# Optimization experiments

Hardware: AMD Instinct MI355X
Metric: run time of the kernel (lower is better)

The kernel has to match this reference:

```python
import jax, jax.numpy as jnp
import numpy as np
from jax import lax

NQ = 5  # qubits
NL = 3  # circuit layers


def conv2d(x, w, b):
    y = lax.conv_general_dilated(x, w, (1, 1), 'SAME',
                                 dimension_numbers=('NCHW', 'OIHW', 'NCHW'))
    return y + b[None, :, None, None]


def batchnorm(x, g, b, eps=1e-5):
    # training-mode batch statistics over (N,H,W), matching nn.BatchNorm2d in train()
    mu = x.mean((0, 2, 3), keepdims=True)
    var = x.var((0, 2, 3), keepdims=True)
    return g[None, :, None, None] * (x - mu) * lax.rsqrt(var + eps) + b[None, :, None, None]


def maxpool2(x):
    return lax.reduce_window(x, -jnp.inf, lax.max, (1, 1, 2, 2), (1, 1, 2, 2), 'VALID')


def _apply_1q(state, U, w):
    # state: (2,)*NQ, wire w is axis w (PennyLane default.qubit ordering)
    s = jnp.tensordot(U, state, axes=([1], [w]))
    return jnp.moveaxis(s, 0, w)


def _cnot(state, c, t):
    s0 = jnp.take(state, 0, axis=c)
    s1 = jnp.take(state, 1, axis=c)
    ta = t if t < c else t - 1
    s1 = jnp.flip(s1, axis=ta)  # X on target when control=1
    return jnp.stack([s0, s1], axis=c)


def _rx(t):
    c, s = jnp.cos(t / 2), jnp.sin(t / 2)
    return jnp.array([[c, -1j * s], [-1j * s, c]], dtype=jnp.complex64)


def _ry(t):
    c, s = jnp.cos(t / 2), jnp.sin(t / 2)
    return jnp.array([[c, -s], [s, c]], dtype=jnp.complex64)


def _rz(t):
    e = jnp.exp(-1j * t / 2)
    z = jnp.zeros((), jnp.complex64)
    return jnp.array([[e, z], [z, jnp.conj(e)]], dtype=jnp.complex64)


def quantum_circuit(inputs, weights):
    # inputs: (5,), weights: (30,)  -> scalar <Z0 Z1 Z2>
    state = jnp.zeros((2,) * NQ, jnp.complex64).at[(0,) * NQ].set(1.0)
    npl = NQ * 2  # weights per layer = 10
    nw = weights.shape[0]
    for l in range(NL):
        for i in range(NQ):
            state = _apply_1q(state, _rx(inputs[i]), i)
        for i in range(NQ):
            state = _apply_1q(state, _ry(weights[(l * npl + i) % nw]), i)
            state = _apply_1q(state, _rz(weights[(l * npl + i + NQ) % nw]), i)
        for i in range(NQ - 1):
            state = _cnot(state, i, i + 1)
        state = _cnot(state, NQ - 1, 0)
    probs = jnp.abs(state) ** 2
    z = jnp.array([1.0, -1.0], jnp.float32)
    sign = z[:, None, None] * z[None, :, None] * z[None, None, :]  # Z on wires 0,1,2
    return jnp.sum(probs * sign[:, :, :, None, None])


def setup_inputs() -> dict:
    key = jax.random.key(0)
    ks = jax.random.split(key, 12)
    d = {}
    d['x'] = jax.random.normal(ks[0], (256, 1, 224, 224), jnp.float32)
    d['conv1_w'] = jax.random.normal(ks[1], (16, 1, 3, 3), jnp.float32) * 0.1
    d['conv1_b'] = jnp.zeros((16,), jnp.float32)
    d['bn1_g'] = jnp.ones((16,), jnp.float32)
    d['bn1_b'] = jnp.zeros((16,), jnp.float32)
    d['conv2_w'] = jax.random.normal(ks[2], (32, 16, 3, 3), jnp.float32) * 0.05
    d['conv2_b'] = jnp.zeros((32,), jnp.float32)
    d['bn2_g'] = jnp.ones((32,), jnp.float32)
    d['bn2_b'] = jnp.zeros((32,), jnp.float32)
    d['conv3_w'] = jax.random.normal(ks[3], (64, 32, 3, 3), jnp.float32) * 0.05
    d['conv3_b'] = jnp.zeros((64,), jnp.float32)
    d['bn3_g'] = jnp.ones((64,), jnp.float32)
    d['bn3_b'] = jnp.zeros((64,), jnp.float32)
    d['fc1_w'] = jax.random.normal(ks[4], (64, 5), jnp.float32) * 0.1   # (in,out)
    d['fc1_b'] = jnp.zeros((5,), jnp.float32)
    d['ln_g'] = jnp.ones((5,), jnp.float32)
    d['ln_b'] = jnp.zeros((5,), jnp.float32)
    d['q_params'] = jax.random.uniform(ks[5], (30,), jnp.float32)
    d['fc2_w'] = jax.random.normal(ks[6], (1, 32), jnp.float32) * 0.5
    d['fc2_b'] = jnp.zeros((32,), jnp.float32)
    d['fc3_w'] = jax.random.normal(ks[7], (32, 2), jnp.float32) * 0.2
    d['fc3_b'] = jnp.zeros((2,), jnp.float32)
    return d


def reference(x, conv1_w, conv1_b, bn1_g, bn1_b, conv2_w, conv2_b, bn2_g, bn2_b,
              conv3_w, conv3_b, bn3_g, bn3_b, fc1_w, fc1_b, ln_g, ln_b,
              q_params, fc2_w, fc2_b, fc3_w, fc3_b):
    h = maxpool2(jax.nn.relu(batchnorm(conv2d(x, conv1_w, conv1_b), bn1_g, bn1_b)))
    h = maxpool2(jax.nn.relu(batchnorm(conv2d(h, conv2_w, conv2_b), bn2_g, bn2_b)))
    h = maxpool2(jax.nn.relu(batchnorm(conv2d(h, conv3_w, conv3_b), bn3_g, bn3_b)))
    # dropout is identity in eval; adaptive avg pool (1,1) + flatten
    h = h.mean((2, 3))                    # (B, 64)
    h = h @ fc1_w + fc1_b                 # (B, 5)
    mu = h.mean(-1, keepdims=True)
    var = h.var(-1, keepdims=True)
    h = ln_g * (h - mu) * lax.rsqrt(var + 1e-5) + ln_b
    q = jax.vmap(lambda inp: quantum_circuit(inp, q_params))(h)  # (B,)
    q = q[:, None].astype(jnp.float32)    # (B, 1)
    h2 = jax.nn.relu(q @ fc2_w + fc2_b)   # (B, 32)
    logits = h2 @ fc3_w + fc3_b           # (B, 2)
    return jax.nn.log_softmax(logits, axis=1)
```

## Files before the change

kernel.cpp:

```cpp
#include <hip/hip_runtime.h>
#include <hip/hip_bf16.h>


typedef _Float16 f16;
typedef _Float16 f16x2 __attribute__((ext_vector_type(2)));
typedef _Float16 f16x4 __attribute__((ext_vector_type(4)));
typedef _Float16 f16x8 __attribute__((ext_vector_type(8)));
typedef float f32x4 __attribute__((ext_vector_type(4)));
typedef float f32x16 __attribute__((ext_vector_type(16)));

#define DEV static __device__ __forceinline__

DEV float wave_sum(float v) {
#pragma unroll
  for (int off = 32; off > 0; off >>= 1) v += __shfl_xor(v, off, 64);
  return v;
}

__global__ __launch_bounds__(256) void repack(const float* __restrict__ w2,
                                              const float* __restrict__ w3,
                                              f16* __restrict__ Bt2,
                                              f16* __restrict__ Bt3) {
  int t = blockIdx.x * 256 + threadIdx.x;
  int T = gridDim.x * 256;
  for (int i = t; i < 32 * 168; i += T) {
    int oc = i / 168, kk = i - oc * 168;
    float v = 0.f;
    if (kk < 144) {
      int tap = kk >> 4, ic = kk & 15;
      v = w2[(oc * 16 + ic) * 9 + tap];
    }
    Bt2[i] = (f16)v;
  }
  for (int i = t; i < 64 * 296; i += T) {
    int oc = i / 296, kk = i - oc * 296;
    float v = 0.f;
    if (kk < 288) {
      int tap = kk / 32, ic = kk & 31;
      v = w3[(oc * 32 + ic) * 9 + tap];
    }
    Bt3[i] = (f16)v;
  }
}

__global__ __launch_bounds__(64) void finalize(const float* __restrict__ banks,
                                               const float* __restrict__ g,
                                               const float* __restrict__ b,
                                               float* __restrict__ scsh, int C,
                                               float inv_n) {
  int c = blockIdx.x, bk = threadIdx.x;
  float s = banks[bk * 2 * C + c];
  float qq = banks[bk * 2 * C + C + c];
  s = wave_sum(s);
  qq = wave_sum(qq);
  if (bk == 0) {
    float mean = s * inv_n;
    float var = qq * inv_n - mean * mean;
    float sc = g[c] * rsqrtf(var + 1e-5f);
    scsh[c] = sc;
    scsh[C + c] = b[c] - mean * sc;
  }
}

__global__ __launch_bounds__(256) void l1_mfma32(const float* __restrict__ x,
                                                 const float* __restrict__ w1,
                                                 float* __restrict__ banks,
                                                 f16* __restrict__ h1raw) {
  __shared__ f16 xA[18 * 240];
  __shared__ f16 xB[18 * 240];
  __shared__ f16 lrow[4 * 3616];
  __shared__ float lstat[32];
  int bid = blockIdx.x;
  int n = bid / 14, band = bid - n * 14;
  int y0 = band * 16;
  int t = threadIdx.x;
  if (t < 32) lstat[t] = 0.f;
  for (int i = t; i < 1008; i += 256) {
    int r = i / 56, k = i - r * 56;
    int y = y0 - 1 + r;
    float4 v = make_float4(0.f, 0.f, 0.f, 0.f);
    if ((unsigned)y < 224u)
      v = *(const float4*)(x + ((size_t)(n * 224 + y)) * 224 + k * 4);
    f16 h0 = (f16)v.x, h1 = (f16)v.y, h2 = (f16)v.z, h3 = (f16)v.w;
    f16* pa = xA + r * 240 + 4 * k + 1;
    pa[0] = h0; pa[1] = h1; pa[2] = h2; pa[3] = h3;
    f16x4 pk = {h0, h1, h2, h3};
    *(f16x4*)(xB + r * 240 + 4 * k) = pk;
  }
  if (t < 18) {
    xA[t * 240 + 0] = (f16)0.f;
    xA[t * 240 + 225] = (f16)0.f;
    xA[t * 240 + 226] = (f16)0.f;
    xB[t * 240 + 224] = (f16)0.f;
    xB[t * 240 + 225] = (f16)0.f;
  }
  __syncthreads();

  int wave = t >> 6, lane = t & 63;
  int g = lane >> 5, m32 = lane & 31;
  int oc = m32 & 15, s = m32 >> 4;

  f16x8 b;
#pragma unroll
  for (int j = 0; j < 8; j++) {
    int ky = 2 * g + (j >> 2), kx = j & 3;
    int kys = ky - s;
    float wv = 0.f;
    if (kx < 3 && kys >= 0 && kys < 3) wv = w1[oc * 9 + kys * 3 + kx];
    b[j] = (f16)wv;
  }

  const f16* abase = (m32 & 1) ? (xB + (m32 - 1)) : (xA + m32);
  f16* myrow = lrow + wave * 3616;
  f16* mrow = myrow + s * 1808;
  f32x16 zero16;
#pragma unroll
  for (int r = 0; r < 16; r++) zero16[r] = 0.f;
  const int bp[8] = {0, 1, 4, 5, 8, 9, 12, 13};
  float ssum = 0.f, ssq = 0.f;

  for (int rp = wave; rp < 8; rp += 4) {
    int r0 = 2 * rp + 2 * g;
    const f16* rbase = abase + r0 * 240;
#pragma unroll
    for (int xt = 0; xt < 7; xt++) {
      const f16* p0 = rbase + xt * 32;
      f16x2 v0 = *(const f16x2*)(p0);
      f16x2 v1 = *(const f16x2*)(p0 + 2);
      f16x2 v2 = *(const f16x2*)(p0 + 240);
      f16x2 v3 = *(const f16x2*)(p0 + 242);
      f16x8 a = {v0[0], v0[1], v1[0], v1[1], v2[0], v2[1], v3[0], v3[1]};
      f32x16 acc = __builtin_amdgcn_mfma_f32_32x32x16_f16(a, b, zero16, 0, 0, 0);
#pragma unroll
      for (int r = 0; r < 16; r++) {
        float v = acc[r];
        ssum += v;
        ssq += v * v;
      }
#pragma unroll
      for (int i = 0; i < 8; i++) {
        float pm = fmaxf(acc[2 * i], acc[2 * i + 1]);
        int pxp = xt * 16 + bp[i] + 2 * g;
        mrow[pxp * 16 + oc] = (f16)pm;
      }
    }
    int ph = band * 8 + rp;
    f16* gdst = h1raw + ((size_t)(n * 112) + ph) * 112 * 16;
    for (int i = lane; i < 224; i += 64) {
      f16x8 va = *(const f16x8*)(myrow + i * 8);
      f16x8 vb = *(const f16x8*)(myrow + 1808 + i * 8);
#pragma unroll
      for (int k = 0; k < 8; k++) va[k] = (va[k] > vb[k]) ? va[k] : vb[k];
      *(f16x8*)(gdst + i * 8) = va;
    }
  }
  ssum += __shfl_xor(ssum, 16, 64);
  ssum += __shfl_xor(ssum, 32, 64);
  ssq += __shfl_xor(ssq, 16, 64);
  ssq += __shfl_xor(ssq, 32, 64);
  if (lane < 16) {
    atomicAdd(&lstat[oc], ssum);
    atomicAdd(&lstat[16 + oc], ssq);
  }
  __syncthreads();
  if (t < 32) atomicAdd(&banks[(bid & 63) * 32 + t], lstat[t]);
}

__global__ __launch_bounds__(256, 3) void l2_gemm(
    const f16* __restrict__ h1, const f16* __restrict__ Btg,
    const float* __restrict__ scsh1, f16* __restrict__ p2,
    float* __restrict__ banks) {
  extern __shared__ char smem[];
  f16* lin = (f16*)smem;
  f16* zslot = (f16*)(smem + 53760);
  float* lstat = (float*)(smem + 53792);
  int bid = blockIdx.x;
  int n = bid / 14, sb = bid - n * 14;
  int t = threadIdx.x;
  int wave = t >> 6, lane = t & 63, q = lane >> 4, wi = lane & 15;
  const int icq = (q & 1) * 8;

  f16x8 breg0[5], breg1[5];
#pragma unroll
  for (int j = 0; j < 5; j++) {
    breg0[j] = *(const f16x8*)(Btg + wi * 168 + j * 32 + q * 8);
    breg1[j] = *(const f16x8*)(Btg + (16 + wi) * 168 + j * 32 + q * 8);
  }

  if (t < 64) lstat[t] = 0.f;
  if (t == 0) {
    f16x8 z = {0, 0, 0, 0, 0, 0, 0, 0};
    *(f16x8*)zslot = z;
  }
#pragma unroll
  for (int k = 0; k < 9; k++) {
    int i = t + k * 256;
    if (i < 2240) {
      int r = i / 224, c = i - r * 224;
      int y = sb * 8 + r - 1;
      f16x8 o = {0, 0, 0, 0, 0, 0, 0, 0};
      if ((unsigned)y < 112u) {
        f16x8 xv =
            *(const f16x8*)(h1 + ((size_t)(n * 112 + y)) * 112 * 16 + c * 8);
        int ch0 = (c & 1) * 8;
#pragma unroll
        for (int e = 0; e < 8; e++) {
          float f = (float)xv[e] * scsh1[ch0 + e] + scsh1[16 + ch0 + e];
          o[e] = (f16)fmaxf(f, 0.f);
        }
      }
      *(f16x8*)(lin + (r * 112 + (c >> 1)) * 24 + (c & 1) * 8) = o;
    }
  }
  __syncthreads();

  f32x4 acc[2][7][2];
#pragma unroll
  for (int rr = 0; rr < 2; rr++)
#pragma unroll
    for (int f = 0; f < 7; f++)
#pragma unroll
      for (int nf = 0; nf < 2; nf++)
#pragma unroll
        for (int r = 0; r < 4; r++) acc[rr][f][nf][r] = 0.f;

#pragma unroll
  for (int j = 0; j < 5; j++) {
    const int tA = 2 * j, tB = 2 * j + 1;
    const int kyA = tA / 3, kxA = tA % 3;
    const int kyB = (tB < 9) ? tB / 3 : 0, kxB = (tB < 9) ? tB % 3 : 0;
    bool hiq = (q >= 2);
    int ky = hiq ? kyB : kyA;
    int kx = hiq ? kxB : kxA;
    f16x8 b0 = breg0[j];
    f16x8 b1 = breg1[j];
    int c0 = wi + kx - 1;
#pragma unroll
    for (int rr = 0; rr < 2; rr++) {
      int ro = 2 * wave + rr;
      const f16* rowbase = lin + (ro + ky) * 112 * 24 + icq;
#pragma unroll
      for (int f = 0; f < 7; f++) {
        int col = c0 + f * 16;
        const f16* ap =
            ((unsigned)col < 112u) ? (rowbase + col * 24) : (const f16*)zslot;
        f16x8 a = *(const f16x8*)ap;
        acc[rr][f][0] =
            __builtin_amdgcn_mfma_f32_16x16x32_f16(a, b0, acc[rr][f][0], 0, 0, 0);
        acc[rr][f][1] =
            __builtin_amdgcn_mfma_f32_16x16x32_f16(a, b1, acc[rr][f][1], 0, 0, 0);
      }
    }
  }

  float tS0 = 0.f, tQ0 = 0.f, tS1 = 0.f, tQ1 = 0.f;
#pragma unroll
  for (int rr = 0; rr < 2; rr++)
#pragma unroll
    for (int f = 0; f < 7; f++)
#pragma unroll
      for (int r = 0; r < 4; r++) {
        float v0 = acc[rr][f][0][r], v1 = acc[rr][f][1][r];
        tS0 += v0; tQ0 += v0 * v0;
        tS1 += v1; tQ1 += v1 * v1;
      }

  {
    int ph = sb * 4 + wave;
    size_t ob = (((size_t)n * 56 + ph) * 56) * 32;
#pragma unroll
    for (int f = 0; f < 7; f++)
#pragma unroll
      for (int nf = 0; nf < 2; nf++) {
        int ch = nf * 16 + wi;
        int pc0 = f * 8 + q * 2;
        float a0 = fmaxf(acc[0][f][nf][0], acc[0][f][nf][1]);
        float a1 = fmaxf(acc[0][f][nf][2], acc[0][f][nf][3]);
        float b0m = fmaxf(acc[1][f][nf][0], acc[1][f][nf][1]);
        float b1m = fmaxf(acc[1][f][nf][2], acc[1][f][nf][3]);
        p2[ob + (size_t)pc0 * 32 + ch] = (f16)fmaxf(a0, b0m);
        p2[ob + (size_t)(pc0 + 1) * 32 + ch] = (f16)fmaxf(a1, b1m);
      }
  }

  tS0 += __shfl_xor(tS0, 16, 64); tS0 += __shfl_xor(tS0, 32, 64);
  tQ0 += __shfl_xor(tQ0, 16, 64); tQ0 += __shfl_xor(tQ0, 32, 64);
  tS1 += __shfl_xor(tS1, 16, 64); tS1 += __shfl_xor(tS1, 32, 64);
  tQ1 += __shfl_xor(tQ1, 16, 64); tQ1 += __shfl_xor(tQ1, 32, 64);
  if (q == 0) {
    atomicAdd(&lstat[wi], tS0);
    atomicAdd(&lstat[16 + wi], tS1);
    atomicAdd(&lstat[32 + wi], tQ0);
    atomicAdd(&lstat[48 + wi], tQ1);
  }
  __syncthreads();
  if (t < 64) {
    int i = t >> 5, c = t & 31;
    atomicAdd(&banks[(bid & 63) * 64 + i * 32 + c], lstat[i * 32 + c]);
  }
}

__global__ __launch_bounds__(256, 2) void l3_gemm(
    const f16* __restrict__ p2, const f16* __restrict__ Btg,
    const float* __restrict__ scsh2, f16* __restrict__ p3,
    float* __restrict__ banks) {
  extern __shared__ char smem[];
  f16* lin = (f16*)smem;
  float* lstat = (float*)(smem + 46400);
  f16* lpool = (f16*)smem;
  int bx = blockIdx.x;
  int n = bx / 7, sb = bx - n * 7;
  int t = threadIdx.x;
  int wave = t >> 6, lane = t & 63, q = lane >> 4, wi = lane & 15;

  f16x8 breg[9][4];
#pragma unroll
  for (int j = 0; j < 9; j++)
#pragma unroll
    for (int h = 0; h < 4; h++)
      breg[j][h] =
          *(const f16x8*)(Btg + (h * 16 + wi) * 296 + j * 32 + q * 8);

  if (t < 128) lstat[t] = 0.f;
#pragma unroll
  for (int k = 0; k < 9; k++) {
    int i = t + k * 256;
    if (i < 2240) {
      int r = i / 224, rem = i - r * 224;
      int c = rem >> 2, cp = rem & 3;
      int y = sb * 8 + r - 1;
      f16x8 o = {0, 0, 0, 0, 0, 0, 0, 0};
      if ((unsigned)y < 56u) {
        f16x8 xv =
            *(const f16x8*)(p2 + (((size_t)(n * 56 + y)) * 56 + c) * 32 +
                            cp * 8);
        int ch0 = cp * 8;
#pragma unroll
        for (int e = 0; e < 8; e++) {
          float f = (float)xv[e] * scsh2[ch0 + e] + scsh2[32 + ch0 + e];
          o[e] = (f16)fmaxf(f, 0.f);
        }
      }
      *(f16x8*)(lin + (r * 58 + 1 + c) * 40 + cp * 8) = o;
    }
  }
  if (t < 80) {
    int r = t / 8, k = t & 7;
    int col = (k < 4) ? 0 : 57, cp = k & 3;
    f16x8 z = {0, 0, 0, 0, 0, 0, 0, 0};
    *(f16x8*)(lin + (r * 58 + col) * 40 + cp * 8) = z;
  }
  __syncthreads();

  int abase[7];
#pragma unroll
  for (int f = 0; f < 7; f++) {
    int pos = wave * 112 + f * 16 + wi;
    int r = pos / 56, w = pos - r * 56;
    abase[f] = (r * 58 + w) * 40 + q * 8;
  }
  f32x4 acc[7][4];
#pragma unroll
  for (int f = 0; f < 7; f++)
#pragma unroll
    for (int h = 0; h < 4; h++)
#pragma unroll
      for (int r = 0; r < 4; r++) acc[f][h][r] = 0.f;

#pragma unroll
  for (int j = 0; j < 9; j++) {
    const int ky = j / 3, kx = j % 3;
#pragma unroll
    for (int f = 0; f < 7; f++) {
      f16x8 a = *(const f16x8*)(lin + abase[f] + (ky * 58 + kx) * 40);
#pragma unroll
      for (int h = 0; h < 4; h++)
        acc[f][h] =
            __builtin_amdgcn_mfma_f32_16x16x32_f16(a, breg[j][h], acc[f][h],
                                                   0, 0, 0);
    }
  }

  float tS[4] = {0.f, 0.f, 0.f, 0.f}, tQ[4] = {0.f, 0.f, 0.f, 0.f};
#pragma unroll
  for (int f = 0; f < 7; f++)
#pragma unroll
    for (int h = 0; h < 4; h++)
#pragma unroll
      for (int r = 0; r < 4; r++) {
        float v = acc[f][h][r];
        tS[h] += v;
        tQ[h] += v * v;
      }
#pragma unroll
  for (int h = 0; h < 4; h++) {
    tS[h] += __shfl_xor(tS[h], 16, 64); tS[h] += __shfl_xor(tS[h], 32, 64);
    tQ[h] += __shfl_xor(tQ[h], 16, 64); tQ[h] += __shfl_xor(tQ[h], 32, 64);
  }
  if (q == 0) {
#pragma unroll
    for (int h = 0; h < 4; h++) {
      atomicAdd(&lstat[h * 16 + wi], tS[h]);
      atomicAdd(&lstat[64 + h * 16 + wi], tQ[h]);
    }
  }
  __syncthreads();

#pragma unroll
  for (int f = 0; f < 7; f++) {
    int pos = wave * 112 + f * 16 + q * 4;
    int r0 = pos / 56, w0 = pos - r0 * 56;
#pragma unroll
    for (int h = 0; h < 4; h++) {
      int ch = h * 16 + wi;
      float m0 = fmaxf(acc[f][h][0], acc[f][h][1]);
      float m1 = fmaxf(acc[f][h][2], acc[f][h][3]);
      lpool[(r0 * 28 + (w0 >> 1)) * 64 + ch] = (f16)m0;
      lpool[(r0 * 28 + (w0 >> 1) + 1) * 64 + ch] = (f16)m1;
    }
  }
  __syncthreads();

  for (int i = t; i < 7168; i += 256) {
    int ch = i & 63, rest = i >> 6;
    int pc = rest % 28, pr = rest / 28;
    float v = fmaxf((float)lpool[((2 * pr) * 28 + pc) * 64 + ch],
                    (float)lpool[((2 * pr + 1) * 28 + pc) * 64 + ch]);
    int gpr = sb * 4 + pr;
    p3[(((size_t)n * 28 + gpr) * 28 + pc) * 64 + ch] = (f16)v;
  }
  if (t < 128) {
    atomicAdd(&banks[(bx & 63) * 128 + t], lstat[t]);
  }
}

__global__ __launch_bounds__(256) void head_pool(
    const f16* __restrict__ p3, const float* __restrict__ scsh3,
    const float* __restrict__ fc1w, const float* __restrict__ fc1b,
    float* __restrict__ featg) {
  int n = blockIdx.x, t = threadIdx.x;
  __shared__ float red[64 * 33];
  __shared__ float meanc[64];
  int oct = t & 7, strip = t >> 3;
  float sc[8], sh[8];
#pragma unroll
  for (int k = 0; k < 8; k++) {
    sc[k] = scsh3[oct * 8 + k];
    sh[k] = scsh3[64 + oct * 8 + k];
  }
  float acc[8];
#pragma unroll
  for (int k = 0; k < 8; k++) acc[k] = 0.f;
  const f16* base = p3 + (size_t)n * 50176 + oct * 8;
  for (int px = strip; px < 784; px += 32) {
    f16x8 v = *(const f16x8*)(base + (size_t)px * 64);
#pragma unroll
    for (int k = 0; k < 8; k++)
      acc[k] += fmaxf((float)v[k] * sc[k] + sh[k], 0.f);
  }
#pragma unroll
  for (int k = 0; k < 8; k++) red[(oct * 8 + k) * 33 + strip] = acc[k];
  __syncthreads();
  if (t < 64) {
    float s = 0.f;
    for (int j = 0; j < 32; j++) s += red[t * 33 + j];
    meanc[t] = s * (1.f / 784.f);
  }
  __syncthreads();
  if (t < 5) {
    float a = fc1b[t];
    for (int i = 0; i < 64; i++) a += meanc[i] * fc1w[i * 5 + t];
    featg[n * 8 + t] = a;
  }
}

template <int W>
DEV void g_rx(float (&sr)[32], float (&si)[32], float c, float s) {
  constexpr int m = 1 << (4 - W);
#pragma unroll
  for (int i0 = 0; i0 < 32; i0++)
    if (!(i0 & m)) {
      int i1 = i0 | m;
      float a0r = sr[i0], a0i = si[i0], a1r = sr[i1], a1i = si[i1];
      sr[i0] = c * a0r + s * a1i;
      si[i0] = c * a0i - s * a1r;
      sr[i1] = s * a0i + c * a1r;
      si[i1] = -s * a0r + c * a1i;
    }
}

template <int W>
DEV void g_ry(float (&sr)[32], float (&si)[32], float c, float s) {
  constexpr int m = 1 << (4 - W);
#pragma unroll
  for (int i0 = 0; i0 < 32; i0++)
    if (!(i0 & m)) {
      int i1 = i0 | m;
      float a0r = sr[i0], a0i = si[i0], a1r = sr[i1], a1i = si[i1];
      sr[i0] = c * a0r - s * a1r;
      si[i0] = c * a0i - s * a1i;
      sr[i1] = s * a0r + c * a1r;
      si[i1] = s * a0i + c * a1i;
    }
}

template <int W>
DEV void g_rz(float (&sr)[32], float (&si)[32], float c, float s) {
  constexpr int m = 1 << (4 - W);
#pragma unroll
  for (int i0 = 0; i0 < 32; i0++)
    if (!(i0 & m)) {
      int i1 = i0 | m;
      float a0r = sr[i0], a0i = si[i0], a1r = sr[i1], a1i = si[i1];
      sr[i0] = c * a0r + s * a0i;
      si[i0] = c * a0i - s * a0r;
      sr[i1] = c * a1r - s * a1i;
      si[i1] = c * a1i + s * a1r;
    }
}

template <int C, int T>
DEV void g_cnot(float (&sr)[32], float (&si)[32]) {
  constexpr int mc = 1 << (4 - C), mt = 1 << (4 - T);
#pragma unroll
  for (int i0 = 0; i0 < 32; i0++)
    if ((i0 & mc) && !(i0 & mt)) {
      int i1 = i0 | mt;
      float tr = sr[i0]; sr[i0] = sr[i1]; sr[i1] = tr;
      float ti = si[i0]; si[i0] = si[i1]; si[i1] = ti;
    }
}

__global__ __launch_bounds__(64) void head_q(
    const float* __restrict__ featg, const float* __restrict__ lng,
    const float* __restrict__ lnb, const float* __restrict__ qp,
    const float* __restrict__ fc2w, const float* __restrict__ fc2b,
    const float* __restrict__ fc3w, const float* __restrict__ fc3b,
    float* __restrict__ out) {
  int n = blockIdx.x * 64 + threadIdx.x;
  float f[5];
#pragma unroll
  for (int i = 0; i < 5; i++) f[i] = featg[n * 8 + i];
  float mu = (f[0] + f[1] + f[2] + f[3] + f[4]) * 0.2f;
  float var = 0.f;
#pragma unroll
  for (int i = 0; i < 5; i++) { float d = f[i] - mu; var += d * d; }
  var *= 0.2f;
  float inv = rsqrtf(var + 1e-5f);
#pragma unroll
  for (int i = 0; i < 5; i++) f[i] = lng[i] * (f[i] - mu) * inv + lnb[i];

  float cx[5], sx[5];
#pragma unroll
  for (int i = 0; i < 5; i++) {
    cx[i] = cosf(0.5f * f[i]);
    sx[i] = sinf(0.5f * f[i]);
  }
  float sr[32], si[32];
#pragma unroll
  for (int i = 0; i < 32; i++) { sr[i] = 0.f; si[i] = 0.f; }
  sr[0] = 1.f;

  for (int l = 0; l < 3; l++) {
    g_rx<0>(sr, si, cx[0], sx[0]);
    g_rx<1>(sr, si, cx[1], sx[1]);
    g_rx<2>(sr, si, cx[2], sx[2]);
    g_rx<3>(sr, si, cx[3], sx[3]);
    g_rx<4>(sr, si, cx[4], sx[4]);
#define WIRE_YZ(I)                                             \
  {                                                            \
    float ty = qp[l * 10 + I];                                 \
    g_ry<I>(sr, si, cosf(0.5f * ty), sinf(0.5f * ty));         \
    float tz = qp[l * 10 + I + 5];                             \
    g_rz<I>(sr, si, cosf(0.5f * tz), sinf(0.5f * tz));         \
  }
    WIRE_YZ(0) WIRE_YZ(1) WIRE_YZ(2) WIRE_YZ(3) WIRE_YZ(4)
#undef WIRE_YZ
    g_cnot<0, 1>(sr, si);
    g_cnot<1, 2>(sr, si);
    g_cnot<2, 3>(sr, si);
    g_cnot<3, 4>(sr, si);
    g_cnot<4, 0>(sr, si);
  }
  float qv = 0.f;
#pragma unroll
  for (int idx = 0; idx < 32; idx++) {
    float p = sr[idx] * sr[idx] + si[idx] * si[idx];
    qv += (__popc(idx & 0x1C) & 1) ? -p : p;
  }
  float l0 = fc3b[0], l1 = fc3b[1];
  for (int j = 0; j < 32; j++) {
    float hv = fmaxf(qv * fc2w[j] + fc2b[j], 0.f);
    l0 += hv * fc3w[j * 2];
    l1 += hv * fc3w[j * 2 + 1];
  }
  float mx = fmaxf(l0, l1);
  float lse = mx + logf(expf(l0 - mx) + expf(l1 - mx));
  out[n * 2 + 0] = l0 - lse;
  out[n * 2 + 1] = l1 - lse;
}

extern "C" void kernel_launch(void* const* d_in, const int* in_sizes, int n_in,
                              void* d_out, int out_size, void* d_ws,
                              size_t ws_size, hipStream_t stream) {
  const float* x    = (const float*)d_in[0];
  const float* w1   = (const float*)d_in[1];
  const float* bn1g = (const float*)d_in[3];
  const float* bn1b = (const float*)d_in[4];
  const float* w2   = (const float*)d_in[5];
  const float* bn2g = (const float*)d_in[7];
  const float* bn2b = (const float*)d_in[8];
  const float* w3   = (const float*)d_in[9];
  const float* bn3g = (const float*)d_in[11];
  const float* bn3b = (const float*)d_in[12];
  const float* fc1w = (const float*)d_in[13];
  const float* fc1b = (const float*)d_in[14];
  const float* lng  = (const float*)d_in[15];
  const float* lnb  = (const float*)d_in[16];
  const float* qp   = (const float*)d_in[17];
  const float* fc2w = (const float*)d_in[18];
  const float* fc2b = (const float*)d_in[19];
  const float* fc3w = (const float*)d_in[20];
  const float* fc3b = (const float*)d_in[21];
  float* out = (float*)d_out;

  char* ws = (char*)d_ws;
  float* banks1 = (float*)ws;
  float* banks2 = (float*)(ws + 8192);
  float* banks3 = (float*)(ws + 24576);
  float* scsh1 = (float*)(ws + 57344);
  float* scsh2 = (float*)(ws + 57472);
  float* scsh3 = (float*)(ws + 57728);
  f16* Bt2 = (f16*)(ws + 58240);
  f16* Bt3 = (f16*)(ws + 68992);
  f16* h1 = (f16*)(ws + 106880);
  f16* p2 = (f16*)(ws + 106880 + 102760448ULL);
  f16* p3 = (f16*)(ws + 106880 + 102760448ULL + 51380224ULL);
  float* featg = banks2;

  hipMemsetAsync(ws, 0, 57344, stream);
  repack<<<16, 256, 0, stream>>>(w2, w3, Bt2, Bt3);
  l1_mfma32<<<3584, 256, 0, stream>>>(x, w1, banks1, h1);
  finalize<<<16, 64, 0, stream>>>(banks1, bn1g, bn1b, scsh1, 16,
                                  1.f / 12845056.f);
  l2_gemm<<<3584, 256, 54048, stream>>>(h1, Bt2, scsh1, p2, banks2);
  finalize<<<32, 64, 0, stream>>>(banks2, bn2g, bn2b, scsh2, 32,
                                  1.f / 3211264.f);
  l3_gemm<<<1792, 256, 46912, stream>>>(p2, Bt3, scsh2, p3, banks3);
  finalize<<<64, 64, 0, stream>>>(banks3, bn3g, bn3b, scsh3, 64,
                                  1.f / 802816.f);
  head_pool<<<256, 256, 0, stream>>>(p3, scsh3, fc1w, fc1b, featg);
  head_q<<<4, 64, 0, stream>>>(featg, lng, lnb, qp, fc2w, fc2b, fc3w, fc3b,
                               out);
}
```

Before: 356.3 us.

## Halve l2_gemm row tile and pool row pairs across waves via LDS

The conv2 GEMM block now covers 4 output rows instead of 8, with each wave computing one row instead of two, and the grid doubles to 7168 blocks. The 2x2 maxpool's vertical max now crosses wave pairs: odd waves write row maxima to an LDS buffer and even waves combine them and store the pooled output. This cuts accumulator registers and shared memory per block so more blocks can be resident. In exchange, the halo rows are reloaded more often relative to useful rows, and there is an extra LDS round trip plus a barrier.

```diff
diff --git a/kernel.cpp b/kernel.cpp
--- a/kernel.cpp
+++ b/kernel.cpp
@@ -172,10 +172,11 @@
     float* __restrict__ banks) {
   extern __shared__ char smem[];
   f16* lin = (f16*)smem;
-  f16* zslot = (f16*)(smem + 53760);
-  float* lstat = (float*)(smem + 53792);
+  f16* zslot = (f16*)(smem + 32256);
+  float* lstat = (float*)(smem + 32288);
+  f16* lpool = (f16*)(smem + 32544);
   int bid = blockIdx.x;
-  int n = bid / 14, sb = bid - n * 14;
+  int n = bid / 28, sb = bid - n * 28;
   int t = threadIdx.x;
   int wave = t >> 6, lane = t & 63, q = lane >> 4, wi = lane & 15;
   const int icq = (q & 1) * 8;
@@ -193,11 +194,11 @@
     *(f16x8*)zslot = z;
   }
 #pragma unroll
-  for (int k = 0; k < 9; k++) {
+  for (int k = 0; k < 6; k++) {
     int i = t + k * 256;
-    if (i < 2240) {
+    if (i < 1344) {
       int r = i / 224, c = i - r * 224;
-      int y = sb * 8 + r - 1;
+      int y = sb * 4 + r - 1;
       f16x8 o = {0, 0, 0, 0, 0, 0, 0, 0};
       if ((unsigned)y < 112u) {
         f16x8 xv =
@@ -214,15 +215,13 @@
   }
   __syncthreads();
 
-  f32x4 acc[2][7][2];
-#pragma unroll
-  for (int rr = 0; rr < 2; rr++)
-#pragma unroll
-    for (int f = 0; f < 7; f++)
-#pragma unroll
-      for (int nf = 0; nf < 2; nf++)
-#pragma unroll
-        for (int r = 0; r < 4; r++) acc[rr][f][nf][r] = 0.f;
+  f32x4 acc[7][2];
+#pragma unroll
+  for (int f = 0; f < 7; f++)
+#pragma unroll
+    for (int nf = 0; nf < 2; nf++)
+#pragma unroll
+      for (int r = 0; r < 4; r++) acc[f][nf][r] = 0.f;
 
 #pragma unroll
   for (int j = 0; j < 5; j++) {
@@ -235,54 +234,29 @@
     f16x8 b0 = breg0[j];
     f16x8 b1 = breg1[j];
     int c0 = wi + kx - 1;
-#pragma unroll
-    for (int rr = 0; rr < 2; rr++) {
-      int ro = 2 * wave + rr;
-      const f16* rowbase = lin + (ro + ky) * 112 * 24 + icq;
-#pragma unroll
-      for (int f = 0; f < 7; f++) {
-        int col = c0 + f * 16;
-        const f16* ap =
-            ((unsigned)col < 112u) ? (rowbase + col * 24) : (const f16*)zslot;
-        f16x8 a = *(const f16x8*)ap;
-        acc[rr][f][0] =
-            __builtin_amdgcn_mfma_f32_16x16x32_f16(a, b0, acc[rr][f][0], 0, 0, 0);
-        acc[rr][f][1] =
-            __builtin_amdgcn_mfma_f32_16x16x32_f16(a, b1, acc[rr][f][1], 0, 0, 0);
-      }
+    const f16* rowbase = lin + (wave + ky) * 112 * 24 + icq;
+#pragma unroll
+    for (int f = 0; f < 7; f++) {
+      int col = c0 + f * 16;
+      const f16* ap =
+          ((unsigned)col < 112u) ? (rowbase + col * 24) : (const f16*)zslot;
+      f16x8 a = *(const f16x8*)ap;
+      acc[f][0] =
+          __builtin_amdgcn_mfma_f32_16x16x32_f16(a, b0, acc[f][0], 0, 0, 0);
+      acc[f][1] =
+          __builtin_amdgcn_mfma_f32_16x16x32_f16(a, b1, acc[f][1], 0, 0, 0);
     }
   }
 
   float tS0 = 0.f, tQ0 = 0.f, tS1 = 0.f, tQ1 = 0.f;
 #pragma unroll
-  for (int rr = 0; rr < 2; rr++)
-#pragma unroll
-    for (int f = 0; f < 7; f++)
-#pragma unroll
-      for (int r = 0; r < 4; r++) {
-        float v0 = acc[rr][f][0][r], v1 = acc[rr][f][1][r];
-        tS0 += v0; tQ0 += v0 * v0;
-        tS1 += v1; tQ1 += v1 * v1;
-      }
-
-  {
-    int ph = sb * 4 + wave;
-    size_t ob = (((size_t)n * 56 + ph) * 56) * 32;
-#pragma unroll
-    for (int f = 0; f < 7; f++)
-#pragma unroll
-      for (int nf = 0; nf < 2; nf++) {
-        int ch = nf * 16 + wi;
-        int pc0 = f * 8 + q * 2;
-        float a0 = fmaxf(acc[0][f][nf][0], acc[0][f][nf][1]);
-        float a1 = fmaxf(acc[0][f][nf][2], acc[0][f][nf][3]);
-        float b0m = fmaxf(acc[1][f][nf][0], acc[1][f][nf][1]);
-        float b1m = fmaxf(acc[1][f][nf][2], acc[1][f][nf][3]);
-        p2[ob + (size_t)pc0 * 32 + ch] = (f16)fmaxf(a0, b0m);
-        p2[ob + (size_t)(pc0 + 1) * 32 + ch] = (f16)fmaxf(a1, b1m);
-      }
-  }
-
+  for (int f = 0; f < 7; f++)
+#pragma unroll
+    for (int r = 0; r < 4; r++) {
+      float v0 = acc[f][0][r], v1 = acc[f][1][r];
+      tS0 += v0; tQ0 += v0 * v0;
+      tS1 += v1; tQ1 += v1 * v1;
+    }
   tS0 += __shfl_xor(tS0, 16, 64); tS0 += __shfl_xor(tS0, 32, 64);
   tQ0 += __shfl_xor(tQ0, 16, 64); tQ0 += __shfl_xor(tQ0, 32, 64);
   tS1 += __shfl_xor(tS1, 16, 64); tS1 += __shfl_xor(tS1, 32, 64);
@@ -293,7 +267,40 @@
     atomicAdd(&lstat[32 + wi], tQ0);
     atomicAdd(&lstat[48 + wi], tQ1);
   }
-  __syncthreads();
+
+  if (wave & 1) {
+#pragma unroll
+    for (int f = 0; f < 7; f++)
+#pragma unroll
+      for (int nf = 0; nf < 2; nf++) {
+        int ch = nf * 16 + wi;
+        int pc0 = f * 8 + q * 2;
+        float m0 = fmaxf(acc[f][nf][0], acc[f][nf][1]);
+        float m1 = fmaxf(acc[f][nf][2], acc[f][nf][3]);
+        lpool[((wave >> 1) * 56 + pc0) * 32 + ch] = (f16)m0;
+        lpool[((wave >> 1) * 56 + pc0 + 1) * 32 + ch] = (f16)m1;
+      }
+  }
+  __syncthreads();
+
+  if (!(wave & 1)) {
+    int ph = sb * 2 + (wave >> 1);
+    size_t ob = (((size_t)n * 56 + ph) * 56) * 32;
+#pragma unroll
+    for (int f = 0; f < 7; f++)
+#pragma unroll
+      for (int nf = 0; nf < 2; nf++) {
+        int ch = nf * 16 + wi;
+        int pc0 = f * 8 + q * 2;
+        float m0 = fmaxf(acc[f][nf][0], acc[f][nf][1]);
+        float m1 = fmaxf(acc[f][nf][2], acc[f][nf][3]);
+        m0 = fmaxf(m0, (float)lpool[((wave >> 1) * 56 + pc0) * 32 + ch]);
+        m1 = fmaxf(m1, (float)lpool[((wave >> 1) * 56 + pc0 + 1) * 32 + ch]);
+        p2[ob + (size_t)pc0 * 32 + ch] = (f16)m0;
+        p2[ob + (size_t)(pc0 + 1) * 32 + ch] = (f16)m1;
+      }
+  }
+
   if (t < 64) {
     int i = t >> 5, c = t & 31;
     atomicAdd(&banks[(bid & 63) * 64 + i * 32 + c], lstat[i * 32 + c]);
@@ -643,7 +650,7 @@
   l1_mfma32<<<3584, 256, 0, stream>>>(x, w1, banks1, h1);
   finalize<<<16, 64, 0, stream>>>(banks1, bn1g, bn1b, scsh1, 16,
                                   1.f / 12845056.f);
-  l2_gemm<<<3584, 256, 54048, stream>>>(h1, Bt2, scsh1, p2, banks2);
+  l2_gemm<<<7168, 256, 39712, stream>>>(h1, Bt2, scsh1, p2, banks2);
   finalize<<<32, 64, 0, stream>>>(banks2, bn2g, bn2b, scsh2, 32,
                                   1.f / 3211264.f);
   l3_gemm<<<1792, 256, 46912, stream>>>(p2, Bt3, scsh2, p3, banks3);
```

After: 343.4 us, median of 2. -3.6%, faster.
